# Performance work log

Measured on AMD Instinct MI355X. Metric: run time of the kernel, lower is better.

Reference implementation:

```python
import jax, jax.numpy as jnp
import numpy as np

U = 100000   # num_users
I = 50000    # num_items
D = 64       # latent_dim_rec
E = 6400000  # nnz of symmetric bipartite adjacency
L = 3        # lightGCN_n_layers
B = 16384    # scoring batch
N = U + I


def setup_inputs() -> dict:
    key = jax.random.key(0)
    ks = jax.random.split(key, 9)
    user_emb = jax.random.normal(ks[0], (U, D), dtype=jnp.float32) * 0.1
    item_emb = jax.random.normal(ks[1], (I, D), dtype=jnp.float32) * 0.1
    user_bias = jnp.zeros((U, 1), dtype=jnp.float32)
    item_bias = jnp.zeros((I, 1), dtype=jnp.float32)
    # edge values mimic symmetric-normalized adjacency (small positive weights)
    vals = jax.random.uniform(ks[2], (E,), dtype=jnp.float32) * (1.0 / 32.0)
    src = jax.random.randint(ks[3], (E,), 0, N, dtype=jnp.int32)
    dst = jax.random.randint(ks[4], (E,), 0, N, dtype=jnp.int32)
    users = jax.random.randint(ks[5], (B,), 0, U, dtype=jnp.int32)
    items = jax.random.randint(ks[6], (B,), 0, I, dtype=jnp.int32)
    return {
        "user_emb": user_emb, "item_emb": item_emb,
        "user_bias": user_bias, "item_bias": item_bias,
        "vals": vals, "src": src, "dst": dst,
        "users": users, "items": items,
    }


def _computer(user_emb, item_emb, vals, src, dst, n_layers):
    # LightGCN.computer(): repeated SpMM (edge-list form) + mean over layers
    all_emb = jnp.concatenate([user_emb, item_emb], axis=0)  # [N, D]
    n = all_emb.shape[0]
    embs = [all_emb]
    for _ in range(n_layers):
        msgs = vals[:, None] * all_emb[src]                   # [E, D] gather
        all_emb = jax.ops.segment_sum(msgs, dst, num_segments=n)  # scatter-add
        embs.append(all_emb)
    light_out = jnp.mean(jnp.stack(embs, axis=1), axis=1)     # [N, D]
    return light_out[:U], light_out[U:]


def reference(user_emb, item_emb, user_bias, item_bias, vals, src, dst, users, items):
    all_users, all_items = _computer(user_emb, item_emb, vals, src, dst, L)
    users_emb = all_users[users]           # [B, D]
    items_emb = all_items[items]           # [B, D]
    users_bias_emb = user_bias[users]      # [B, 1]
    items_bias_emb = item_bias[items]      # [B, 1]
    inner_pro = (users_bias_emb + items_bias_emb) + users_emb * items_emb  # [B, D]
    gamma = jnp.sum(inner_pro, axis=1)     # [B]
    return gamma
```

## Files before the change

### kernel.cpp

```cpp
#include <hip/hip_runtime.h>
#include <hip/hip_fp16.h>
#include <hip/hip_fp8.h>
#include <stdint.h>

#define U_N 100000
#define I_N 50000
#define D_DIM 64
#define E_N 6400000
#define B_N 16384
#define N_N 150000
#define BKN 128
#define NB 1172
#define CAPB 6144
#define CHUNK_A 6250
#define PAIRS 586

#define S0_F 512.0f
#define S1_F 1024.0f
#define S2_F 8192.0f

typedef unsigned long long ull;
typedef __attribute__((ext_vector_type(2))) float f32x2;

__device__ __forceinline__ unsigned short pack_fp8(float a, float b) {
#if __has_builtin(__builtin_amdgcn_cvt_pk_fp8_f32)
    return (unsigned short)(__builtin_amdgcn_cvt_pk_fp8_f32(a, b, 0, false) & 0xFFFF);
#else
    __hip_fp8_e4m3 qa(a), qb(b);
    return (unsigned short)((unsigned)qa.__x | ((unsigned)qb.__x << 8));
#endif
}
__device__ __forceinline__ f32x2 unpack_fp8(unsigned short u) {
#if __has_builtin(__builtin_amdgcn_cvt_pk_f32_fp8)
    return __builtin_amdgcn_cvt_pk_f32_fp8((int)(unsigned)u, false);
#else
    __hip_fp8_e4m3 qa, qb;
    qa.__x = (unsigned char)(u & 0xFF);
    qb.__x = (unsigned char)(u >> 8);
    f32x2 r; r[0] = (float)qa; r[1] = (float)qb; return r;
#endif
}

__global__ __launch_bounds__(256) void to_fp8(const float2* __restrict__ ue2,
                                              const float2* __restrict__ ie2,
                                              unsigned short* __restrict__ b80) {
    const int total = N_N * 32;
    const int utot = U_N * 32;
    for (int i = blockIdx.x * blockDim.x + threadIdx.x; i < total;
         i += gridDim.x * blockDim.x) {
        float2 x = (i < utot) ? ue2[i] : ie2[i - utot];
        b80[i] = pack_fp8(x.x * S0_F, x.y * S0_F);
    }
}

__global__ __launch_bounds__(1024) void phaseA(const int* __restrict__ src,
                                               const int* __restrict__ dst,
                                               const float* __restrict__ vals,
                                               int* __restrict__ bcur,
                                               ull* __restrict__ staging) {
    __shared__ int hist[NB];
    __shared__ int delta[NB];
    __shared__ ull recs[CHUNK_A];
    __shared__ int wsum[10];
    const int tid = threadIdx.x;
    const int beg = blockIdx.x * CHUNK_A;

    for (int i = tid; i < NB; i += 1024) hist[i] = 0;
    __syncthreads();
    for (int e = tid; e < CHUNK_A; e += 1024)
        atomicAdd(&hist[((unsigned)dst[beg + e]) >> 7], 1);
    __syncthreads();

    int e0 = 0, e1 = 0, s = 0;
    if (tid < PAIRS) { e0 = hist[2 * tid]; e1 = hist[2 * tid + 1]; s = e0 + e1; }
    int incl = s;
#pragma unroll
    for (int off = 1; off < 64; off <<= 1) {
        int v = __shfl_up(incl, off, 64);
        if ((tid & 63) >= off) incl += v;
    }
    if ((tid & 63) == 63 && (tid >> 6) < 10) wsum[tid >> 6] = incl;
    __syncthreads();
    if (tid == 0) {
        int run = 0;
        for (int w = 0; w < 10; ++w) { int t = wsum[w]; wsum[w] = run; run += t; }
    }
    __syncthreads();
    if (tid < PAIRS) {
        int excl = wsum[tid >> 6] + incl - s;
        int b0 = 2 * tid, b1 = 2 * tid + 1;
        int g0 = e0 ? atomicAdd(&bcur[b0], e0) : 0;
        int g1 = e1 ? atomicAdd(&bcur[b1], e1) : 0;
        delta[b0] = b0 * CAPB + g0 - excl;
        delta[b1] = b1 * CAPB + g1 - (excl + e0);
        hist[b0] = excl;
        hist[b1] = excl + e0;
    }
    __syncthreads();

    for (int e = tid; e < CHUNK_A; e += 1024) {
        int d = dst[beg + e];
        unsigned b = ((unsigned)d) >> 7;
        unsigned short hb = __half_as_ushort(__float2half(vals[beg + e]));
        ull rec = ((ull)hb << 36) | ((ull)(unsigned)d << 18)
                | (ull)(unsigned)src[beg + e];
        int lpos = atomicAdd(&hist[b], 1);
        recs[lpos] = rec;
    }
    __syncthreads();

    for (int i = tid; i < CHUNK_A; i += 1024) {
        ull rec = recs[i];
        unsigned d = (unsigned)(rec >> 18) & 0x3FFFFu;
        unsigned b = d >> 7;
        staging[(size_t)(delta[b] + i)] = rec;
    }
}

__global__ __launch_bounds__(256) void phaseB(const ull* __restrict__ staging,
                                              const int* __restrict__ bcur,
                                              unsigned* __restrict__ csr_src,
                                              __half* __restrict__ csr_val,
                                              int* __restrict__ row_ptr,
                                              unsigned short* __restrict__ row_len) {
    __shared__ ull recs[CAPB];
    __shared__ int hist[BKN];
    __shared__ int curs[BKN];
    const int b = blockIdx.x;
    const int cnt = bcur[b];
    const int sbase = b * CAPB;
    for (int i = threadIdx.x; i < BKN; i += 256) hist[i] = 0;
    __syncthreads();
    for (int i = threadIdx.x; i < cnt; i += 256) {
        ull rec = staging[sbase + i];
        recs[i] = rec;
        atomicAdd(&hist[(int)((rec >> 18) & 0x7Fu)], 1);
    }
    __syncthreads();
    if (threadIdx.x < 64) {
        int lane = threadIdx.x;
        int carry = 0;
#pragma unroll
        for (int c = 0; c < BKN; c += 64) {
            int x = hist[c + lane];
            int inc = x;
#pragma unroll
            for (int off = 1; off < 64; off <<= 1) {
                int v = __shfl_up(inc, off, 64);
                if (lane >= off) inc += v;
            }
            int excl = carry + inc - x;
            int node = b * BKN + c + lane;
            if (node < N_N) {
                row_ptr[node] = sbase + excl;
                row_len[node] = (unsigned short)x;
            }
            curs[c + lane] = excl;
            carry += __shfl(inc, 63, 64);
        }
    }
    __syncthreads();
    for (int i = threadIdx.x; i < cnt; i += 256) {
        ull rec = recs[i];
        int local = (int)((rec >> 18) & 0x7Fu);
        int pos = sbase + atomicAdd(&curs[local], 1);
        csr_src[pos] = (unsigned)((rec & 0x3FFFFu) << 6);
        csr_val[pos] = __ushort_as_half((unsigned short)(rec >> 36));
    }
}

template<int M>
__device__ __forceinline__ void gather_fma8(const char* __restrict__ eb8,
                                            int2 (*recs)[64], int wid, int j0,
                                            int hlf, int col2,
                                            float& accx, float& accy) {
    unsigned short g[M];
    float v[M];
#pragma unroll
    for (int k = 0; k < M; ++k) {
        int2 r = recs[wid][j0 + 2 * k + hlf];
        v[k] = __int_as_float(r.y);
        g[k] = *(const unsigned short*)(eb8 + (size_t)(unsigned)r.x + col2);
    }
#pragma unroll
    for (int k = 0; k < M; ++k) {
        f32x2 f = unpack_fp8(g[k]);
        accx += f[0] * v[k];
        accy += f[1] * v[k];
    }
}

__device__ __forceinline__ void spmm_row8(const char* __restrict__ eb8,
                                          const unsigned* __restrict__ csr_src,
                                          const __half* __restrict__ csr_val,
                                          int2 (*recs)[64], int wid, int lane,
                                          int hlf, int col2,
                                          int beg, int end,
                                          float& accx, float& accy) {
    for (int base = beg; base < end; base += 64) {
        int2 rec;
        if (base + lane < end) {
            rec.x = (int)csr_src[base + lane];
            rec.y = __float_as_int(__half2float(csr_val[base + lane]));
        } else {
            rec = make_int2(0, 0);
        }
        recs[wid][lane] = rec;
        int cnt = min(64, end - base);
        int j0 = 0;
        for (; j0 + 32 <= cnt; j0 += 32)
            gather_fma8<16>(eb8, recs, wid, j0, hlf, col2, accx, accy);
        for (; j0 < cnt; j0 += 16)
            gather_fma8<8>(eb8, recs, wid, j0, hlf, col2, accx, accy);
    }
}

__global__ __launch_bounds__(256) void spmm8(const unsigned short* __restrict__ tbl,
                                             unsigned short* __restrict__ out8,
                                             float out_scale,
                                             const int* __restrict__ row_ptr,
                                             const unsigned short* __restrict__ row_len,
                                             const unsigned* __restrict__ csr_src,
                                             const __half* __restrict__ csr_val) {
    __shared__ int2 recs[4][64];
    const int wid = threadIdx.x >> 6;
    const int lane = threadIdx.x & 63;
    const int hlf = lane >> 5;
    const int col = lane & 31;
    int row = blockIdx.x * 4 + wid;
    if (row >= N_N) return;
    int beg = row_ptr[row];
    int end = beg + row_len[row];
    float accx = 0.f, accy = 0.f;
    spmm_row8((const char*)tbl, csr_src, csr_val, recs, wid, lane, hlf,
              col * 2, beg, end, accx, accy);
    accx += __shfl_xor(accx, 32, 64);
    accy += __shfl_xor(accy, 32, 64);
    if (lane < 32)
        out8[(size_t)row * 32 + col] = pack_fp8(accx * out_scale, accy * out_scale);
}

__global__ __launch_bounds__(256) void batch_final(const unsigned short* __restrict__ b81,
                                                   const unsigned short* __restrict__ b82,
                                                   const float2* __restrict__ ue2,
                                                   const float2* __restrict__ ie2,
                                                   const int* __restrict__ users,
                                                   const int* __restrict__ items,
                                                   const int* __restrict__ row_ptr,
                                                   const unsigned short* __restrict__ row_len,
                                                   const unsigned* __restrict__ csr_src,
                                                   const __half* __restrict__ csr_val,
                                                   float2* __restrict__ su2,
                                                   float2* __restrict__ si2) {
    __shared__ int2 recs[4][64];
    const int wid = threadIdx.x >> 6;
    const int lane = threadIdx.x & 63;
    const int hlf = lane >> 5;
    const int col = lane & 31;
    int r = blockIdx.x * 4 + wid;
    if (r >= 2 * B_N) return;
    bool isu = (r < B_N);
    int node = isu ? users[r] : U_N + items[r - B_N];
    int beg = row_ptr[node];
    int end = beg + row_len[node];
    float accx = 0.f, accy = 0.f;
    spmm_row8((const char*)b82, csr_src, csr_val, recs, wid, lane, hlf,
              col * 2, beg, end, accx, accy);
    accx += __shfl_xor(accx, 32, 64);
    accy += __shfl_xor(accy, 32, 64);
    if (lane < 32) {
        size_t toff = (size_t)node * 32 + col;
        f32x2 e1 = unpack_fp8(b81[toff]);
        f32x2 e2 = unpack_fp8(b82[toff]);
        float2 e0 = isu ? ue2[toff] : ie2[(size_t)(node - U_N) * 32 + col];
        float2 o;
        o.x = e0.x + e1[0] * (1.0f / S1_F) + (e2[0] + accx) * (1.0f / S2_F);
        o.y = e0.y + e1[1] * (1.0f / S1_F) + (e2[1] + accy) * (1.0f / S2_F);
        if (isu) su2[(size_t)r * 32 + col] = o;
        else     si2[(size_t)(r - B_N) * 32 + col] = o;
    }
}

__global__ __launch_bounds__(256) void gamma_kernel(const float* __restrict__ su,
                                                    const float* __restrict__ si,
                                                    const float* __restrict__ ub,
                                                    const float* __restrict__ ib,
                                                    const int* __restrict__ users,
                                                    const int* __restrict__ items,
                                                    float* __restrict__ out) {
    int b = blockIdx.x * 4 + (threadIdx.x >> 6);
    int lane = threadIdx.x & 63;
    if (b >= B_N) return;
    float p = su[(size_t)b * D_DIM + lane] * si[(size_t)b * D_DIM + lane];
#pragma unroll
    for (int off = 32; off > 0; off >>= 1) p += __shfl_xor(p, off, 64);
    if (lane == 0) {
        float bias = ub[users[b]] + ib[items[b]];
        out[b] = p * (1.0f / 16.0f) + 64.0f * bias;
    }
}

extern "C" void kernel_launch(void* const* d_in, const int* in_sizes, int n_in,
                              void* d_out, int out_size, void* d_ws, size_t ws_size,
                              hipStream_t stream) {
    const float* user_emb  = (const float*)d_in[0];
    const float* item_emb  = (const float*)d_in[1];
    const float* user_bias = (const float*)d_in[2];
    const float* item_bias = (const float*)d_in[3];
    const float* vals      = (const float*)d_in[4];
    const int*   src       = (const int*)d_in[5];
    const int*   dst       = (const int*)d_in[6];
    const int*   users     = (const int*)d_in[7];
    const int*   items     = (const int*)d_in[8];
    float* out = (float*)d_out;

    char* ws = (char*)d_ws;
    size_t off = 0;
    auto alloc = [&](size_t bytes) -> void* {
        void* p = ws + off;
        off += (bytes + 255) & ~(size_t)255;
        return p;
    };
    const size_t SLOTS = (size_t)NB * CAPB;
    const size_t TBL = (size_t)N_N * 32;
    unsigned short* b80 = (unsigned short*)alloc(sizeof(short) * TBL);
    unsigned short* b81 = (unsigned short*)alloc(sizeof(short) * TBL);
    unsigned short* b82 = (unsigned short*)alloc(sizeof(short) * TBL);
    float*  su      = (float*)alloc(sizeof(float) * (size_t)B_N * D_DIM);
    float*  si      = (float*)alloc(sizeof(float) * (size_t)B_N * D_DIM);
    int*    row_ptr = (int*)alloc(sizeof(int) * N_N);
    unsigned short* row_len = (unsigned short*)alloc(sizeof(short) * N_N);
    int*    bcur    = (int*)alloc(sizeof(int) * NB);
    ull*    staging = (ull*)alloc(sizeof(ull) * SLOTS);
    unsigned* csr_src = (unsigned*)alloc(sizeof(unsigned) * SLOTS);
    __half* csr_val = (__half*)alloc(sizeof(__half) * SLOTS);

    hipMemsetAsync(bcur, 0, sizeof(int) * NB, stream);

    to_fp8<<<2048, 256, 0, stream>>>((const float2*)user_emb,
                                     (const float2*)item_emb, b80);
    phaseA<<<1024, 1024, 0, stream>>>(src, dst, vals, bcur, staging);
    phaseB<<<NB, 256, 0, stream>>>(staging, bcur, csr_src, csr_val,
                                   row_ptr, row_len);

    spmm8<<<(N_N + 3) / 4, 256, 0, stream>>>(b80, b81, S1_F / S0_F,
                                             row_ptr, row_len, csr_src, csr_val);
    spmm8<<<(N_N + 3) / 4, 256, 0, stream>>>(b81, b82, S2_F / S1_F,
                                             row_ptr, row_len, csr_src, csr_val);
    batch_final<<<(2 * B_N) / 4, 256, 0, stream>>>(b81, b82,
                                                   (const float2*)user_emb,
                                                   (const float2*)item_emb,
                                                   users, items,
                                                   row_ptr, row_len, csr_src, csr_val,
                                                   (float2*)su, (float2*)si);

    gamma_kernel<<<B_N / 4, 256, 0, stream>>>(su, si, user_bias, item_bias,
                                              users, items, out);
}
```

Measured before the change: 341.1 us.

## Split SpMM into two source-range passes for cache locality of gathered table

Each CSR row is partitioned by source id (below/above a split point) in phaseB, and each SpMM layer becomes two kernels that gather from one half of the fp8 embedding table at a time. The first pass stores an fp16 partial sum, which the second pass adds before quantizing. The aim is to keep each pass's gather working set (about half the table) resident in L2/LLC. phaseA also preloads its per-thread edges into registers instead of rereading dst, and the tail gather uses a smaller 4-wide step. This costs an extra launch per layer, an fp16 partial read/write of the full node table, and extra rounding from the fp16 partial.

```diff
diff --git a/kernel.cpp b/kernel.cpp
--- a/kernel.cpp
+++ b/kernel.cpp
@@ -12,8 +12,11 @@
 #define BKN 128
 #define NB 1172
 #define CAPB 6144
-#define CHUNK_A 6250
+#define CHUNK_A 6144
+#define NE_A 6
+#define NBLK_A 1042
 #define PAIRS 586
+#define T_SPLIT 75000
 
 #define S0_F 512.0f
 #define S1_F 1024.0f
@@ -65,10 +68,19 @@
     const int tid = threadIdx.x;
     const int beg = blockIdx.x * CHUNK_A;
 
+    int d[NE_A];
+    bool ok[NE_A];
+#pragma unroll
+    for (int i = 0; i < NE_A; ++i) {
+        int e = beg + tid + i * 1024;
+        ok[i] = (e < E_N);
+        d[i] = ok[i] ? dst[e] : 0;
+    }
     for (int i = tid; i < NB; i += 1024) hist[i] = 0;
     __syncthreads();
-    for (int e = tid; e < CHUNK_A; e += 1024)
-        atomicAdd(&hist[((unsigned)dst[beg + e]) >> 7], 1);
+#pragma unroll
+    for (int i = 0; i < NE_A; ++i)
+        if (ok[i]) atomicAdd(&hist[(unsigned)d[i] >> 7], 1);
     __syncthreads();
 
     int e0 = 0, e1 = 0, s = 0;
@@ -98,22 +110,35 @@
     }
     __syncthreads();
 
-    for (int e = tid; e < CHUNK_A; e += 1024) {
-        int d = dst[beg + e];
-        unsigned b = ((unsigned)d) >> 7;
-        unsigned short hb = __half_as_ushort(__float2half(vals[beg + e]));
-        ull rec = ((ull)hb << 36) | ((ull)(unsigned)d << 18)
-                | (ull)(unsigned)src[beg + e];
-        int lpos = atomicAdd(&hist[b], 1);
-        recs[lpos] = rec;
-    }
-    __syncthreads();
-
-    for (int i = tid; i < CHUNK_A; i += 1024) {
-        ull rec = recs[i];
-        unsigned d = (unsigned)(rec >> 18) & 0x3FFFFu;
-        unsigned b = d >> 7;
-        staging[(size_t)(delta[b] + i)] = rec;
+    int sv[NE_A];
+    float vv[NE_A];
+#pragma unroll
+    for (int i = 0; i < NE_A; ++i) {
+        int e = beg + tid + i * 1024;
+        sv[i] = ok[i] ? src[e] : 0;
+        vv[i] = ok[i] ? vals[e] : 0.f;
+    }
+    ull rec[NE_A];
+#pragma unroll
+    for (int i = 0; i < NE_A; ++i) {
+        unsigned short hb = __half_as_ushort(__float2half(vv[i]));
+        rec[i] = ((ull)hb << 36) | ((ull)(unsigned)d[i] << 18)
+               | (ull)(unsigned)sv[i];
+    }
+    int lpos[NE_A];
+#pragma unroll
+    for (int i = 0; i < NE_A; ++i)
+        if (ok[i]) lpos[i] = atomicAdd(&hist[(unsigned)d[i] >> 7], 1);
+#pragma unroll
+    for (int i = 0; i < NE_A; ++i)
+        if (ok[i]) recs[lpos[i]] = rec[i];
+    __syncthreads();
+
+    const int lim = min(CHUNK_A, E_N - beg);
+    for (int i = tid; i < lim; i += 1024) {
+        ull r = recs[i];
+        unsigned dd = (unsigned)(r >> 18) & 0x3FFFFu;
+        staging[(size_t)(delta[dd >> 7] + i)] = r;
     }
 }
 
@@ -122,26 +147,28 @@
                                               unsigned* __restrict__ csr_src,
                                               __half* __restrict__ csr_val,
                                               int* __restrict__ row_ptr,
-                                              unsigned short* __restrict__ row_len) {
+                                              unsigned* __restrict__ rowinfo) {
     __shared__ ull recs[CAPB];
-    __shared__ int hist[BKN];
-    __shared__ int curs[BKN];
+    __shared__ int hist[256];
+    __shared__ int curs[256];
     const int b = blockIdx.x;
     const int cnt = bcur[b];
     const int sbase = b * CAPB;
-    for (int i = threadIdx.x; i < BKN; i += 256) hist[i] = 0;
+    hist[threadIdx.x] = 0;
     __syncthreads();
     for (int i = threadIdx.x; i < cnt; i += 256) {
         ull rec = staging[sbase + i];
         recs[i] = rec;
-        atomicAdd(&hist[(int)((rec >> 18) & 0x7Fu)], 1);
+        int local = (int)((rec >> 18) & 0x7Fu);
+        int tile = ((unsigned)(rec & 0x3FFFFu) >= T_SPLIT) ? 1 : 0;
+        atomicAdd(&hist[local * 2 + tile], 1);
     }
     __syncthreads();
     if (threadIdx.x < 64) {
         int lane = threadIdx.x;
         int carry = 0;
 #pragma unroll
-        for (int c = 0; c < BKN; c += 64) {
+        for (int c = 0; c < 256; c += 64) {
             int x = hist[c + lane];
             int inc = x;
 #pragma unroll
@@ -149,22 +176,30 @@
                 int v = __shfl_up(inc, off, 64);
                 if (lane >= off) inc += v;
             }
-            int excl = carry + inc - x;
-            int node = b * BKN + c + lane;
+            curs[c + lane] = carry + inc - x;
+            carry += __shfl(inc, 63, 64);
+        }
+#pragma unroll
+        for (int c = 0; c < 128; c += 64) {
+            int n = c + lane;
+            int base_ = curs[2 * n];
+            int lo = curs[2 * n + 1] - base_;
+            int nxt = (n == 127) ? cnt : curs[2 * n + 2];
+            int node = b * BKN + n;
             if (node < N_N) {
-                row_ptr[node] = sbase + excl;
-                row_len[node] = (unsigned short)x;
+                row_ptr[node] = sbase + base_;
+                rowinfo[node] = (unsigned)lo | ((unsigned)(nxt - base_) << 16);
             }
-            curs[c + lane] = excl;
-            carry += __shfl(inc, 63, 64);
         }
     }
     __syncthreads();
     for (int i = threadIdx.x; i < cnt; i += 256) {
         ull rec = recs[i];
         int local = (int)((rec >> 18) & 0x7Fu);
-        int pos = sbase + atomicAdd(&curs[local], 1);
-        csr_src[pos] = (unsigned)((rec & 0x3FFFFu) << 6);
+        unsigned srcid = (unsigned)(rec & 0x3FFFFu);
+        int tile = (srcid >= T_SPLIT) ? 1 : 0;
+        int pos = sbase + atomicAdd(&curs[local * 2 + tile], 1);
+        csr_src[pos] = srcid << 6;
         csr_val[pos] = __ushort_as_half((unsigned short)(rec >> 36));
     }
 }
@@ -210,18 +245,22 @@
         int j0 = 0;
         for (; j0 + 32 <= cnt; j0 += 32)
             gather_fma8<16>(eb8, recs, wid, j0, hlf, col2, accx, accy);
-        for (; j0 < cnt; j0 += 16)
+        int rem = cnt - j0;
+        if (rem > 16) {
             gather_fma8<8>(eb8, recs, wid, j0, hlf, col2, accx, accy);
-    }
-}
-
-__global__ __launch_bounds__(256) void spmm8(const unsigned short* __restrict__ tbl,
-                                             unsigned short* __restrict__ out8,
-                                             float out_scale,
-                                             const int* __restrict__ row_ptr,
-                                             const unsigned short* __restrict__ row_len,
-                                             const unsigned* __restrict__ csr_src,
-                                             const __half* __restrict__ csr_val) {
+            j0 += 16; rem -= 16;
+        }
+        if (rem > 8)      gather_fma8<8>(eb8, recs, wid, j0, hlf, col2, accx, accy);
+        else if (rem > 0) gather_fma8<4>(eb8, recs, wid, j0, hlf, col2, accx, accy);
+    }
+}
+
+__global__ __launch_bounds__(256) void spmm8_p1(const unsigned short* __restrict__ tbl,
+                                                __half2* __restrict__ partial,
+                                                const int* __restrict__ row_ptr,
+                                                const unsigned* __restrict__ rowinfo,
+                                                const unsigned* __restrict__ csr_src,
+                                                const __half* __restrict__ csr_val) {
     __shared__ int2 recs[4][64];
     const int wid = threadIdx.x >> 6;
     const int lane = threadIdx.x & 63;
@@ -230,14 +269,46 @@
     int row = blockIdx.x * 4 + wid;
     if (row >= N_N) return;
     int beg = row_ptr[row];
-    int end = beg + row_len[row];
+    int lo = (int)(rowinfo[row] & 0xFFFFu);
     float accx = 0.f, accy = 0.f;
     spmm_row8((const char*)tbl, csr_src, csr_val, recs, wid, lane, hlf,
-              col * 2, beg, end, accx, accy);
+              col * 2, beg, beg + lo, accx, accy);
     accx += __shfl_xor(accx, 32, 64);
     accy += __shfl_xor(accy, 32, 64);
     if (lane < 32)
-        out8[(size_t)row * 32 + col] = pack_fp8(accx * out_scale, accy * out_scale);
+        partial[(size_t)row * 32 + col] = __floats2half2_rn(accx, accy);
+}
+
+__global__ __launch_bounds__(256) void spmm8_p2(const unsigned short* __restrict__ tbl,
+                                                const __half2* __restrict__ partial,
+                                                unsigned short* __restrict__ out8,
+                                                float out_scale,
+                                                const int* __restrict__ row_ptr,
+                                                const unsigned* __restrict__ rowinfo,
+                                                const unsigned* __restrict__ csr_src,
+                                                const __half* __restrict__ csr_val) {
+    __shared__ int2 recs[4][64];
+    const int wid = threadIdx.x >> 6;
+    const int lane = threadIdx.x & 63;
+    const int hlf = lane >> 5;
+    const int col = lane & 31;
+    int row = blockIdx.x * 4 + wid;
+    if (row >= N_N) return;
+    int beg = row_ptr[row];
+    unsigned info = rowinfo[row];
+    int lo = (int)(info & 0xFFFFu);
+    int tot = (int)(info >> 16);
+    float accx = 0.f, accy = 0.f;
+    spmm_row8((const char*)tbl, csr_src, csr_val, recs, wid, lane, hlf,
+              col * 2, beg + lo, beg + tot, accx, accy);
+    accx += __shfl_xor(accx, 32, 64);
+    accy += __shfl_xor(accy, 32, 64);
+    if (lane < 32) {
+        __half2 p = partial[(size_t)row * 32 + col];
+        out8[(size_t)row * 32 + col] =
+            pack_fp8((accx + __low2float(p)) * out_scale,
+                     (accy + __high2float(p)) * out_scale);
+    }
 }
 
 __global__ __launch_bounds__(256) void batch_final(const unsigned short* __restrict__ b81,
@@ -247,7 +318,7 @@
                                                    const int* __restrict__ users,
                                                    const int* __restrict__ items,
                                                    const int* __restrict__ row_ptr,
-                                                   const unsigned short* __restrict__ row_len,
+                                                   const unsigned* __restrict__ rowinfo,
                                                    const unsigned* __restrict__ csr_src,
                                                    const __half* __restrict__ csr_val,
                                                    float2* __restrict__ su2,
@@ -262,7 +333,7 @@
     bool isu = (r < B_N);
     int node = isu ? users[r] : U_N + items[r - B_N];
     int beg = row_ptr[node];
-    int end = beg + row_len[node];
+    int end = beg + (int)(rowinfo[node] >> 16);
     float accx = 0.f, accy = 0.f;
     spmm_row8((const char*)b82, csr_src, csr_val, recs, wid, lane, hlf,
               col * 2, beg, end, accx, accy);
@@ -326,10 +397,11 @@
     unsigned short* b80 = (unsigned short*)alloc(sizeof(short) * TBL);
     unsigned short* b81 = (unsigned short*)alloc(sizeof(short) * TBL);
     unsigned short* b82 = (unsigned short*)alloc(sizeof(short) * TBL);
+    __half* p16     = (__half*)alloc(sizeof(__half) * (size_t)N_N * D_DIM);
     float*  su      = (float*)alloc(sizeof(float) * (size_t)B_N * D_DIM);
     float*  si      = (float*)alloc(sizeof(float) * (size_t)B_N * D_DIM);
     int*    row_ptr = (int*)alloc(sizeof(int) * N_N);
-    unsigned short* row_len = (unsigned short*)alloc(sizeof(short) * N_N);
+    unsigned* rowinfo = (unsigned*)alloc(sizeof(unsigned) * N_N);
     int*    bcur    = (int*)alloc(sizeof(int) * NB);
     ull*    staging = (ull*)alloc(sizeof(ull) * SLOTS);
     unsigned* csr_src = (unsigned*)alloc(sizeof(unsigned) * SLOTS);
@@ -339,19 +411,25 @@
 
     to_fp8<<<2048, 256, 0, stream>>>((const float2*)user_emb,
                                      (const float2*)item_emb, b80);
-    phaseA<<<1024, 1024, 0, stream>>>(src, dst, vals, bcur, staging);
+    phaseA<<<NBLK_A, 1024, 0, stream>>>(src, dst, vals, bcur, staging);
     phaseB<<<NB, 256, 0, stream>>>(staging, bcur, csr_src, csr_val,
-                                   row_ptr, row_len);
-
-    spmm8<<<(N_N + 3) / 4, 256, 0, stream>>>(b80, b81, S1_F / S0_F,
-                                             row_ptr, row_len, csr_src, csr_val);
-    spmm8<<<(N_N + 3) / 4, 256, 0, stream>>>(b81, b82, S2_F / S1_F,
-                                             row_ptr, row_len, csr_src, csr_val);
+                                   row_ptr, rowinfo);
+
+    spmm8_p1<<<(N_N + 3) / 4, 256, 0, stream>>>(b80, (__half2*)p16,
+                                                row_ptr, rowinfo, csr_src, csr_val);
+    spmm8_p2<<<(N_N + 3) / 4, 256, 0, stream>>>(b80, (const __half2*)p16, b81,
+                                                S1_F / S0_F,
+                                                row_ptr, rowinfo, csr_src, csr_val);
+    spmm8_p1<<<(N_N + 3) / 4, 256, 0, stream>>>(b81, (__half2*)p16,
+                                                row_ptr, rowinfo, csr_src, csr_val);
+    spmm8_p2<<<(N_N + 3) / 4, 256, 0, stream>>>(b81, (const __half2*)p16, b82,
+                                                S2_F / S1_F,
+                                                row_ptr, rowinfo, csr_src, csr_val);
     batch_final<<<(2 * B_N) / 4, 256, 0, stream>>>(b81, b82,
                                                    (const float2*)user_emb,
                                                    (const float2*)item_emb,
                                                    users, items,
-                                                   row_ptr, row_len, csr_src, csr_val,
+                                                   row_ptr, rowinfo, csr_src, csr_val,
                                                    (float2*)su, (float2*)si);
 
     gamma_kernel<<<B_N / 4, 256, 0, stream>>>(su, si, user_bias, item_bias,
```

New measurement: 442.9 us. 29.9% more time.
